# Kernel optimization log

Hardware: AMD Instinct MI355X
Metric: run time of the kernel (lower is better)

The kernel has to match this reference:

```python
import jax, jax.numpy as jnp
import numpy as np

B, C, H, W = 16, 256, 32, 32
AD, SC, R = 16, 32, 4


def _conv1x1(x, w, b):
    # x: [B,Cin,H,W], w: [Cout,Cin], b: [Cout]
    return jnp.einsum('oc,bchw->bohw', w, x) + b[None, :, None, None]


def setup_inputs() -> dict:
    key = jax.random.key(0)
    ks = jax.random.split(key, 12)
    p = lambda k, shape: (jax.random.normal(k, shape, dtype=jnp.float32) * 0.02)
    return {
        'x': jax.random.normal(ks[0], (B, C, H, W), dtype=jnp.float32),
        'fc1_w': p(ks[1], (C // R, C)), 'fc1_b': jnp.zeros((C // R,), jnp.float32),
        'fc2_w': p(ks[2], (C, C // R)), 'fc2_b': jnp.zeros((C,), jnp.float32),
        'qkv_w': p(ks[3], (AD * 2 + SC, SC)), 'qkv_b': jnp.zeros((AD * 2 + SC,), jnp.float32),
        'proj_w': p(ks[4], (SC, SC)), 'proj_b': jnp.zeros((SC,), jnp.float32),
        'ffn1_w': p(ks[5], (4 * C, C)), 'ffn1_b': jnp.zeros((4 * C,), jnp.float32),
        'ffn2_w': p(ks[6], (C, 4 * C)), 'ffn2_b': jnp.zeros((C,), jnp.float32),
    }


def reference(x, fc1_w, fc1_b, fc2_w, fc2_b, qkv_w, qkv_b, proj_w, proj_b,
              ffn1_w, ffn1_b, ffn2_w, ffn2_b):
    # --- DynamicChannelSelect: SE gate then channel split ---
    s = x.mean(axis=(2, 3), keepdims=True)                       # [B,C,1,1]
    s = jax.nn.relu(_conv1x1(s, fc1_w, fc1_b))
    s = jax.nn.sigmoid(_conv1x1(s, fc2_w, fc2_b))
    xg = x * s
    attn_part, non_attn_part = xg[:, :SC], xg[:, SC:]

    # --- SHSA: single-head self-attention on SC channels ---
    qkv = _conv1x1(attn_part, qkv_w, qkv_b)                      # [B,2*AD+SC,H,W]
    q = qkv[:, :AD].reshape(B, AD, H * W)
    k = qkv[:, AD:2 * AD].reshape(B, AD, H * W)
    v = qkv[:, 2 * AD:].reshape(B, SC, H * W)
    scale = AD ** -0.5
    attn = jax.nn.softmax(jnp.einsum('bcn,bcm->bnm', q, k) * scale, axis=-1)  # [B,N,N]
    out = jnp.einsum('bcm,bnm->bcn', v, attn).reshape(B, SC, H, W)
    attn_out = _conv1x1(out, proj_w, proj_b)

    # --- concat + 1x1-conv FFN ---
    y = jnp.concatenate([attn_out, non_attn_part], axis=1)       # [B,C,H,W]
    h = jax.nn.relu(_conv1x1(y, ffn1_w, ffn1_b))                 # [B,4C,H,W]
    return _conv1x1(h, ffn2_w, ffn2_b)                           # [B,C,H,W]
```

## Files before the change

### kernel.cpp

```cpp
#include <hip/hip_runtime.h>
#include <cstdint>
#include <cstddef>

#define BB 16
#define CC 256
#define NP 1024

typedef __attribute__((ext_vector_type(8))) short bf16x8;
typedef __attribute__((ext_vector_type(4))) float f32x4;
typedef unsigned short u16;

__device__ __forceinline__ u16 f2bf(float f) {
    union { float f; uint32_t u; } v; v.f = f;
    uint32_t u = v.u;
    return (u16)((u + 0x7FFFu + ((u >> 16) & 1u)) >> 16);
}

__global__ __launch_bounds__(256)
void se_mean_conv_kernel(const float* __restrict__ x, float* __restrict__ s_mean,
                         const float* __restrict__ w1, u16* __restrict__ d1,
                         const float* __restrict__ w2, u16* __restrict__ d2) {
    int blk = blockIdx.x;
    int t = threadIdx.x;
    if (blk < BB * CC) {
        const float* p = x + (size_t)blk * NP;
        float4 v = *(const float4*)(p + t * 4);
        float s = (v.x + v.y) + (v.z + v.w);
#pragma unroll
        for (int off = 32; off; off >>= 1) s += __shfl_down(s, off, 64);
        __shared__ float red[4];
        if ((t & 63) == 0) red[t >> 6] = s;
        __syncthreads();
        if (t == 0) s_mean[blk] = (red[0] + red[1] + red[2] + red[3]) * (1.0f / NP);
    } else {
        int blk2 = blk - BB * CC;
        const float* src = (blk2 < 256) ? w1 : w2;
        u16* dst = (blk2 < 256) ? d1 : d2;
        int i = ((blk2 & 255) * 256 + t) * 4;
        float4 v = *(const float4*)(src + i);
        ushort4 o;
        o.x = f2bf(v.x); o.y = f2bf(v.y); o.z = f2bf(v.z); o.w = f2bf(v.w);
        *(ushort4*)(dst + i) = o;
    }
}

__global__ __launch_bounds__(256)
void se_mlp_kernel(const float* __restrict__ s_mean,
                   const float* __restrict__ fc1_w, const float* __restrict__ fc1_b,
                   const float* __restrict__ fc2_w, const float* __restrict__ fc2_b,
                   float* __restrict__ sig) {
    int b = blockIdx.x, t = threadIdx.x;
    __shared__ float sm[256];
    __shared__ float part[4][64];
    __shared__ float h1[64];
    sm[t] = s_mean[b * 256 + t];
    __syncthreads();
    int to = t & 63, g = t >> 6;
    float a = 0.f;
#pragma unroll 8
    for (int c = 0; c < 64; ++c) a += fc1_w[to * 256 + g * 64 + c] * sm[g * 64 + c];
    part[g][to] = a;
    __syncthreads();
    if (t < 64) h1[t] = fmaxf(part[0][t] + part[1][t] + part[2][t] + part[3][t] + fc1_b[t], 0.f);
    __syncthreads();
    float acc = fc2_b[t];
#pragma unroll 8
    for (int j = 0; j < 64; ++j) acc += fc2_w[t * 64 + j] * h1[j];
    sig[b * 256 + t] = 1.f / (1.f + __expf(-acc));
}

__global__ __launch_bounds__(256)
void scale_transpose_qkv_kernel(const float* __restrict__ x, const float* __restrict__ sig,
                                const float* __restrict__ qW, const float* __restrict__ qB,
                                u16* __restrict__ ygt, u16* __restrict__ Qt,
                                u16* __restrict__ Kt, u16* __restrict__ Vb) {
    int nt = blockIdx.x, ct = blockIdx.y, b = blockIdx.z;
    __shared__ float tile[64][65];
    __shared__ float ws[64 * 32];
    __shared__ float bs[64];
    __shared__ float vtile[32][64];
    __shared__ float sig_l[64];
    int t = threadIdx.x;
    const float* Xb = x + ((size_t)b * CC + ct * 64) * NP + nt * 64;
    if (t < 64) sig_l[t] = sig[b * 256 + ct * 64 + t];
    if (ct == 0) {
        for (int e = t; e < 2048; e += 256) ws[e] = qW[e];
        if (t < 64) bs[t] = qB[t];
    }
#pragma unroll
    for (int p = 0; p < 4; ++p) {
        int e = t + p * 256;
        int c = e >> 4, n4 = (e & 15) * 4;
        float4 v = *(const float4*)&Xb[(size_t)c * NP + n4];
        tile[c][n4] = v.x; tile[c][n4 + 1] = v.y; tile[c][n4 + 2] = v.z; tile[c][n4 + 3] = v.w;
    }
    __syncthreads();
    u16* Yb = ygt + ((size_t)b * NP + nt * 64) * CC + ct * 64;
#pragma unroll
    for (int p = 0; p < 4; ++p) {
        int e = t + p * 256;
        int n = e >> 4, c4 = (e & 15) * 4;
        if (ct * 64 + c4 >= 32) {
            ushort4 o;
            o.x = f2bf(tile[c4][n] * sig_l[c4]);
            o.y = f2bf(tile[c4 + 1][n] * sig_l[c4 + 1]);
            o.z = f2bf(tile[c4 + 2][n] * sig_l[c4 + 2]);
            o.w = f2bf(tile[c4 + 3][n] * sig_l[c4 + 3]);
            *(ushort4*)&Yb[(size_t)n * CC + c4] = o;
        }
    }
    if (ct == 0) {
        int nn = t & 63, g = t >> 6;
        int n = nt * 64 + nn;
        float xs[32];
#pragma unroll
        for (int c = 0; c < 32; ++c) xs[c] = tile[c][nn] * sig_l[c];
        float acc[16];
#pragma unroll
        for (int oc = 0; oc < 16; ++oc) {
            int o = g * 16 + oc;
            float a = bs[o];
#pragma unroll
            for (int c = 0; c < 32; ++c) a += ws[o * 32 + c] * xs[c];
            acc[oc] = a;
        }
        if (g == 0) {
            u16* qr = Qt + ((size_t)b * NP + n) * 32;
            ushort4 z4; z4.x = 0; z4.y = 0; z4.z = 0; z4.w = 0;
#pragma unroll
            for (int j = 0; j < 16; j += 4) {
                ushort4 o4;
                o4.x = f2bf(acc[j] * 0.25f);     o4.y = f2bf(acc[j + 1] * 0.25f);
                o4.z = f2bf(acc[j + 2] * 0.25f); o4.w = f2bf(acc[j + 3] * 0.25f);
                *(ushort4*)&qr[j] = o4;
            }
            *(ushort4*)&qr[16] = z4; *(ushort4*)&qr[20] = z4;
            *(ushort4*)&qr[24] = z4; *(ushort4*)&qr[28] = z4;
        } else if (g == 1) {
            u16* kr = Kt + ((size_t)b * NP + n) * 32;
            ushort4 z4; z4.x = 0; z4.y = 0; z4.z = 0; z4.w = 0;
#pragma unroll
            for (int j = 0; j < 16; j += 4) {
                ushort4 k4;
                k4.x = f2bf(acc[j]);     k4.y = f2bf(acc[j + 1]);
                k4.z = f2bf(acc[j + 2]); k4.w = f2bf(acc[j + 3]);
                *(ushort4*)&kr[j] = k4;
            }
            *(ushort4*)&kr[16] = z4; *(ushort4*)&kr[20] = z4;
            *(ushort4*)&kr[24] = z4; *(ushort4*)&kr[28] = z4;
        } else {
#pragma unroll
            for (int oc = 0; oc < 16; ++oc) vtile[(g - 2) * 16 + oc][nn] = acc[oc];
        }
        __syncthreads();
        for (int e = t; e < 2048; e += 256) {
            int c = e >> 6, nn2 = e & 63;
            Vb[(size_t)b * 32 * NP + (size_t)c * NP + nt * 64 + nn2] = f2bf(vtile[c][nn2]);
        }
    }
}

__global__ __launch_bounds__(256)
void attn_mfma_kernel(const u16* __restrict__ Qt, const u16* __restrict__ Kt,
                      const u16* __restrict__ Vb,
                      const float* __restrict__ proj_w, const float* __restrict__ proj_b,
                      u16* __restrict__ ygt) {
    int b = blockIdx.x & 15;
    int n0 = (blockIdx.x >> 4) * 16;
    __shared__ __align__(16) u16 P_lds[4][16][40];
    __shared__ float al_lds[4][16];
    __shared__ float sm_lds[4][16];
    __shared__ float sl_lds[4][16];
    __shared__ float O_lds[4][16][33];
    __shared__ float pw_s[32][33];
    __shared__ float pb_s[32];
    int t = threadIdx.x;
    int w = t >> 6, lane = t & 63;
    int q = lane >> 4, idx = lane & 15;

    for (int e = t; e < 1024; e += 256) pw_s[e >> 5][e & 31] = proj_w[e];
    if (t < 32) pb_s[t] = proj_b[t];
    __syncthreads();

    const u16* Qb = Qt + (size_t)b * NP * 32;
    const u16* Kb = Kt + (size_t)b * NP * 32;
    const u16* Vp = Vb + (size_t)b * 32 * NP;

    int nrow = n0 + idx;
    bf16x8 aq = *(const bf16x8*)&Qb[(size_t)nrow * 32 + q * 8];

    f32x4 O0 = {0.f, 0.f, 0.f, 0.f}, O1 = {0.f, 0.f, 0.f, 0.f};
    float m_run[4] = {-1e30f, -1e30f, -1e30f, -1e30f};
    float l_run[4] = {0.f, 0.f, 0.f, 0.f};

    int mbase = w * 256;
    for (int m0 = mbase; m0 < mbase + 256; m0 += 32) {
        bf16x8 bk0 = *(const bf16x8*)&Kb[(size_t)(m0 + idx) * 32 + q * 8];
        bf16x8 bk1 = *(const bf16x8*)&Kb[(size_t)(m0 + 16 + idx) * 32 + q * 8];
        bf16x8 va0 = *(const bf16x8*)&Vp[(size_t)idx * NP + m0 + q * 8];
        bf16x8 va1 = *(const bf16x8*)&Vp[(size_t)(16 + idx) * NP + m0 + q * 8];
        f32x4 z = {0.f, 0.f, 0.f, 0.f};
        f32x4 S0 = __builtin_amdgcn_mfma_f32_16x16x32_bf16(aq, bk0, z, 0, 0, 0);
        f32x4 S1 = __builtin_amdgcn_mfma_f32_16x16x32_bf16(aq, bk1, z, 0, 0, 0);
        float mx[4], p0[4], p1[4], alpha[4];
#pragma unroll
        for (int r = 0; r < 4; ++r) mx[r] = fmaxf(S0[r], S1[r]);
#pragma unroll
        for (int off = 1; off < 16; off <<= 1)
#pragma unroll
            for (int r = 0; r < 4; ++r) mx[r] = fmaxf(mx[r], __shfl_xor(mx[r], off, 64));
#pragma unroll
        for (int r = 0; r < 4; ++r) {
            float nm = fmaxf(m_run[r], mx[r]);
            alpha[r] = __expf(m_run[r] - nm);
            m_run[r] = nm;
            p0[r] = __expf(S0[r] - nm);
            p1[r] = __expf(S1[r] - nm);
        }
#pragma unroll
        for (int r = 0; r < 4; ++r) {
            float s = p0[r] + p1[r];
#pragma unroll
            for (int off = 1; off < 16; off <<= 1) s += __shfl_xor(s, off, 64);
            l_run[r] = l_run[r] * alpha[r] + s;
        }
#pragma unroll
        for (int r = 0; r < 4; ++r) {
            P_lds[w][q * 4 + r][idx]      = f2bf(p0[r]);
            P_lds[w][q * 4 + r][idx + 16] = f2bf(p1[r]);
        }
        if (idx == 0) {
#pragma unroll
            for (int r = 0; r < 4; ++r) al_lds[w][q * 4 + r] = alpha[r];
        }
        float an = al_lds[w][idx];
#pragma unroll
        for (int r = 0; r < 4; ++r) { O0[r] *= an; O1[r] *= an; }
        bf16x8 pf = *(const bf16x8*)&P_lds[w][idx][q * 8];
        O0 = __builtin_amdgcn_mfma_f32_16x16x32_bf16(va0, pf, O0, 0, 0, 0);
        O1 = __builtin_amdgcn_mfma_f32_16x16x32_bf16(va1, pf, O1, 0, 0, 0);
    }
    if (idx == 0) {
#pragma unroll
        for (int r = 0; r < 4; ++r) {
            sm_lds[w][q * 4 + r] = m_run[r];
            sl_lds[w][q * 4 + r] = l_run[r];
        }
    }
#pragma unroll
    for (int r = 0; r < 4; ++r) {
        O_lds[w][idx][q * 4 + r]      = O0[r];
        O_lds[w][idx][q * 4 + r + 16] = O1[r];
    }
    __syncthreads();

#pragma unroll
    for (int p = 0; p < 2; ++p) {
        int el = t + p * 256;
        int row = el >> 5, col = el & 31;
        float m0_ = sm_lds[0][row], m1 = sm_lds[1][row], m2 = sm_lds[2][row], m3 = sm_lds[3][row];
        float gm = fmaxf(fmaxf(m0_, m1), fmaxf(m2, m3));
        float e0 = __expf(m0_ - gm), e1 = __expf(m1 - gm);
        float e2 = __expf(m2 - gm), e3 = __expf(m3 - gm);
        float linv = 1.f / (sl_lds[0][row] * e0 + sl_lds[1][row] * e1 +
                            sl_lds[2][row] * e2 + sl_lds[3][row] * e3);
        O_lds[0][row][col] = (O_lds[0][row][col] * e0 + O_lds[1][row][col] * e1 +
                              O_lds[2][row][col] * e2 + O_lds[3][row][col] * e3) * linv;
    }
    __syncthreads();

    {
        int row = (w << 2) + q;
        float o0 = pb_s[idx], o1 = pb_s[idx + 16];
#pragma unroll
        for (int c = 0; c < 32; ++c) {
            float xv = O_lds[0][row][c];
            o0 += pw_s[idx][c] * xv;
            o1 += pw_s[idx + 16][c] * xv;
        }
        u16* yrow = ygt + ((size_t)b * NP + n0 + row) * CC;
        yrow[idx]      = f2bf(o0);
        yrow[idx + 16] = f2bf(o1);
    }
}

__global__ __launch_bounds__(512, 2)
void ffn_fused_kernel(const u16* __restrict__ w1b, const u16* __restrict__ w2b,
                      const u16* __restrict__ ygt,
                      const float* __restrict__ bias1, const float* __restrict__ bias2,
                      float* __restrict__ out) {
    __shared__ __align__(16) u16 Ys[4][64][64];
    __shared__ __align__(16) u16 Hs[2][64][64];
    __shared__ __align__(16) u16 W2s[2][256][64];
    __shared__ float Bs1[1024];
    int t = threadIdx.x;
    int w = t >> 6, lane = t & 63;
    int q = lane >> 4, idx = lane & 15;
    int srow = lane >> 3;
    int gch = (lane & 7) ^ srow;
    int n0 = blockIdx.x * 64;
    int rot = blockIdx.x & 7;
    int hh = w >> 2, wm = w & 3;

#define ISSUE_W2S(sc_)                                                                     \
    {                                                                                      \
        _Pragma("unroll")                                                                  \
        for (int e = 0; e < 8; ++e) {                                                      \
            int hh2 = e >> 2, rnd = e & 3;                                                 \
            int rw = rnd * 64 + w * 8;                                                     \
            __builtin_amdgcn_global_load_lds(                                              \
                (const __attribute__((address_space(1))) void*)(w2b + (size_t)(rw + srow) * 1024 + (sc_) * 128 + hh2 * 64 + gch * 8), \
                (__attribute__((address_space(3))) void*)(&W2s[hh2][rw][0]),               \
                16, 0, 0);                                                                 \
        }                                                                                  \
    }

#define LOAD_AF(dst, sc_)                                                                  \
    {                                                                                      \
        const u16* a1 = w1b + ((size_t)((sc_) * 128 + w * 16 + idx)) * CC;                 \
        _Pragma("unroll")                                                                  \
        for (int s = 0; s < 8; ++s) dst[s] = *(const bf16x8*)(a1 + s * 32 + q * 8);        \
    }

#pragma unroll
    for (int e = 0; e < 4; ++e) {
        __builtin_amdgcn_global_load_lds(
            (const __attribute__((address_space(1))) void*)(ygt + (size_t)(n0 + w * 8 + srow) * CC + e * 64 + gch * 8),
            (__attribute__((address_space(3))) void*)(&Ys[e][w * 8][0]),
            16, 0, 0);
    }
    Bs1[t] = bias1[t];
    Bs1[t + 512] = bias1[t + 512];

    f32x4 oacc[4][4];
#pragma unroll
    for (int f = 0; f < 4; ++f)
#pragma unroll
        for (int j = 0; j < 4; ++j) { f32x4 z = {0.f, 0.f, 0.f, 0.f}; oacc[f][j] = z; }

    ISSUE_W2S(rot)
    bf16x8 af[8];
    LOAD_AF(af, rot)
    __syncthreads();

    for (int it = 0; it < 8; ++it) {
        int sc  = (it + rot) & 7;
        int scn = (it + 1 + rot) & 7;
        bf16x8 afn[8];
        if (it + 1 < 8) LOAD_AF(afn, scn)

        f32x4 hacc[4];
#pragma unroll
        for (int j = 0; j < 4; ++j) { f32x4 z = {0.f, 0.f, 0.f, 0.f}; hacc[j] = z; }
#pragma unroll
        for (int s = 0; s < 8; ++s) {
            int kb = s >> 1, h2 = s & 1;
#pragma unroll
            for (int j = 0; j < 4; ++j) {
                bf16x8 yb = *(const bf16x8*)&Ys[kb][j * 16 + idx][(((q + 4 * h2) ^ (idx & 7)) * 8)];
                hacc[j] = __builtin_amdgcn_mfma_f32_16x16x32_bf16(af[s], yb, hacc[j], 0, 0, 0);
            }
        }

        int mb = sc * 128 + w * 16 + q * 4;
        float b0 = Bs1[mb], b1v = Bs1[mb + 1], b2v = Bs1[mb + 2], b3v = Bs1[mb + 3];
        int chk_hi = wm * 2 + (q >> 1);
#pragma unroll
        for (int j = 0; j < 4; ++j) {
            int n = j * 16 + idx;
            int chk = chk_hi ^ (n & 7);
            uint32_t lo = (uint32_t)f2bf(fmaxf(hacc[j][0] + b0, 0.f)) |
                          ((uint32_t)f2bf(fmaxf(hacc[j][1] + b1v, 0.f)) << 16);
            uint32_t hi = (uint32_t)f2bf(fmaxf(hacc[j][2] + b2v, 0.f)) |
                          ((uint32_t)f2bf(fmaxf(hacc[j][3] + b3v, 0.f)) << 16);
            uint32_t* hp = (uint32_t*)&Hs[hh][n][chk * 8 + (q & 1) * 4];
            hp[0] = lo; hp[1] = hi;
        }
        __syncthreads();

#pragma unroll
        for (int s2 = 0; s2 < 2; ++s2) {
            bf16x8 a2f[4];
#pragma unroll
            for (int f = 0; f < 4; ++f)
                a2f[f] = *(const bf16x8*)&W2s[hh][wm * 64 + f * 16 + idx][(((q + 4 * s2) ^ (idx & 7)) * 8)];
#pragma unroll
            for (int j = 0; j < 4; ++j) {
                bf16x8 hb = *(const bf16x8*)&Hs[hh][j * 16 + idx][(((q + 4 * s2) ^ (idx & 7)) * 8)];
#pragma unroll
                for (int f = 0; f < 4; ++f)
                    oacc[f][j] = __builtin_amdgcn_mfma_f32_16x16x32_bf16(a2f[f], hb, oacc[f][j], 0, 0, 0);
            }
        }
        __syncthreads();

        if (it + 1 < 8) {
            ISSUE_W2S(scn)
#pragma unroll
            for (int s = 0; s < 8; ++s) af[s] = afn[s];
        }
    }
#undef ISSUE_W2S
#undef LOAD_AF

    float* R = (float*)&W2s[0][0][0];
    if (w >= 4) {
#pragma unroll
        for (int f = 0; f < 4; ++f)
#pragma unroll
            for (int j = 0; j < 4; ++j)
#pragma unroll
                for (int r = 0; r < 4; ++r)
                    R[(wm * 64 + f * 16 + q * 4 + r) * 64 + j * 16 + idx] = oacc[f][j][r];
    }
    __syncthreads();
    if (w < 4) {
        int b = n0 >> 10, nnb = n0 & 1023;
#pragma unroll
        for (int f = 0; f < 4; ++f) {
            int m2 = wm * 64 + f * 16 + q * 4;
            float c0 = bias2[m2], c1 = bias2[m2 + 1], c2 = bias2[m2 + 2], c3 = bias2[m2 + 3];
#pragma unroll
            for (int j = 0; j < 4; ++j) {
                int col = j * 16 + idx;
                const float* Rp = &R[m2 * 64 + col];
                float* p = out + ((size_t)b * CC + m2) * NP + nnb + col;
                f32x4 v = oacc[f][j];
                p[0]      = v.x + c0 + Rp[0];
                p[NP]     = v.y + c1 + Rp[64];
                p[2 * NP] = v.z + c2 + Rp[128];
                p[3 * NP] = v.w + c3 + Rp[192];
            }
        }
    }
}

extern "C" void kernel_launch(void* const* d_in, const int* in_sizes, int n_in,
                              void* d_out, int out_size, void* d_ws, size_t ws_size,
                              hipStream_t stream) {
    const float* x      = (const float*)d_in[0];
    const float* fc1_w  = (const float*)d_in[1];
    const float* fc1_b  = (const float*)d_in[2];
    const float* fc2_w  = (const float*)d_in[3];
    const float* fc2_b  = (const float*)d_in[4];
    const float* qkv_w  = (const float*)d_in[5];
    const float* qkv_b  = (const float*)d_in[6];
    const float* proj_w = (const float*)d_in[7];
    const float* proj_b = (const float*)d_in[8];
    const float* ffn1_w = (const float*)d_in[9];
    const float* ffn1_b = (const float*)d_in[10];
    const float* ffn2_w = (const float*)d_in[11];
    const float* ffn2_b = (const float*)d_in[12];
    float* out = (float*)d_out;

    u16* w1b = (u16*)d_ws;
    u16* w2b = w1b + 262144;
    u16* ygt = w2b + 262144;
    u16* scratch = ygt + (size_t)BB * NP * CC;
    float* s_mean = (float*)scratch;
    float* sig    = s_mean + BB * CC;
    u16* Qt = (u16*)(sig + BB * CC);
    u16* Kt = Qt + (size_t)BB * NP * 32;
    u16* Vb = Kt + (size_t)BB * NP * 32;

    se_mean_conv_kernel<<<BB * CC + 512, 256, 0, stream>>>(x, s_mean, ffn1_w, w1b, ffn2_w, w2b);
    se_mlp_kernel<<<BB, 256, 0, stream>>>(s_mean, fc1_w, fc1_b, fc2_w, fc2_b, sig);
    scale_transpose_qkv_kernel<<<dim3(16, 4, BB), 256, 0, stream>>>(
        x, sig, qkv_w, qkv_b, ygt, Qt, Kt, Vb);
    attn_mfma_kernel<<<BB * 64, 256, 0, stream>>>(Qt, Kt, Vb, proj_w, proj_b, ygt);

    ffn_fused_kernel<<<256, 512, 0, stream>>>(w1b, w2b, ygt, ffn1_b, ffn2_b, out);
}
```

Baseline: 161.3 us.

## Retile FFN1 warp work to 32x32 and prefetch W1 fragments after H barrier

Each warp now computes a 32-row by 32-column tile of the first FFN GEMM (two W1 row groups against half the pixels) instead of 16 rows by all 64 pixels. This halves the Y fragment LDS reads per MFMA, since each Y fragment now feeds two MFMAs. The next chunk's W1 fragments are loaded right after the H barrier, behind a scheduling barrier, rather than before the first GEMM, so the double-buffered afn registers are no longer needed. The cost is that W1 global load latency now has to be hidden by the second GEMM alone. Register pressure from the af array stays about the same.

```diff
diff --git a/kernel.cpp b/kernel.cpp
--- a/kernel.cpp
+++ b/kernel.cpp
@@ -301,6 +301,7 @@
     int n0 = blockIdx.x * 64;
     int rot = blockIdx.x & 7;
     int hh = w >> 2, wm = w & 3;
+    int nh = hh * 32;
 
 #define ISSUE_W2S(sc_)                                                                     \
     {                                                                                      \
@@ -315,11 +316,14 @@
         }                                                                                  \
     }
 
-#define LOAD_AF(dst, sc_)                                                                  \
+#define LOAD_AF(sc_)                                                                       \
     {                                                                                      \
-        const u16* a1 = w1b + ((size_t)((sc_) * 128 + w * 16 + idx)) * CC;                 \
+        const u16* a1 = w1b + ((size_t)((sc_) * 128 + wm * 32 + idx)) * CC;                \
         _Pragma("unroll")                                                                  \
-        for (int s = 0; s < 8; ++s) dst[s] = *(const bf16x8*)(a1 + s * 32 + q * 8);        \
+        for (int i2 = 0; i2 < 2; ++i2)                                                     \
+            _Pragma("unroll")                                                              \
+            for (int s = 0; s < 8; ++s)                                                    \
+                af[i2][s] = *(const bf16x8*)(a1 + (size_t)i2 * 16 * CC + s * 32 + q * 8);  \
     }
 
 #pragma unroll
@@ -339,44 +343,55 @@
         for (int j = 0; j < 4; ++j) { f32x4 z = {0.f, 0.f, 0.f, 0.f}; oacc[f][j] = z; }
 
     ISSUE_W2S(rot)
-    bf16x8 af[8];
-    LOAD_AF(af, rot)
+    bf16x8 af[2][8];
+    LOAD_AF(rot)
     __syncthreads();
 
     for (int it = 0; it < 8; ++it) {
         int sc  = (it + rot) & 7;
         int scn = (it + 1 + rot) & 7;
-        bf16x8 afn[8];
-        if (it + 1 < 8) LOAD_AF(afn, scn)
-
-        f32x4 hacc[4];
-#pragma unroll
-        for (int j = 0; j < 4; ++j) { f32x4 z = {0.f, 0.f, 0.f, 0.f}; hacc[j] = z; }
+
+        f32x4 hacc[2][2];
+#pragma unroll
+        for (int i2 = 0; i2 < 2; ++i2)
+#pragma unroll
+            for (int j = 0; j < 2; ++j) { f32x4 z = {0.f, 0.f, 0.f, 0.f}; hacc[i2][j] = z; }
 #pragma unroll
         for (int s = 0; s < 8; ++s) {
             int kb = s >> 1, h2 = s & 1;
 #pragma unroll
-            for (int j = 0; j < 4; ++j) {
-                bf16x8 yb = *(const bf16x8*)&Ys[kb][j * 16 + idx][(((q + 4 * h2) ^ (idx & 7)) * 8)];
-                hacc[j] = __builtin_amdgcn_mfma_f32_16x16x32_bf16(af[s], yb, hacc[j], 0, 0, 0);
-            }
-        }
-
-        int mb = sc * 128 + w * 16 + q * 4;
-        float b0 = Bs1[mb], b1v = Bs1[mb + 1], b2v = Bs1[mb + 2], b3v = Bs1[mb + 3];
-        int chk_hi = wm * 2 + (q >> 1);
-#pragma unroll
-        for (int j = 0; j < 4; ++j) {
-            int n = j * 16 + idx;
-            int chk = chk_hi ^ (n & 7);
-            uint32_t lo = (uint32_t)f2bf(fmaxf(hacc[j][0] + b0, 0.f)) |
-                          ((uint32_t)f2bf(fmaxf(hacc[j][1] + b1v, 0.f)) << 16);
-            uint32_t hi = (uint32_t)f2bf(fmaxf(hacc[j][2] + b2v, 0.f)) |
-                          ((uint32_t)f2bf(fmaxf(hacc[j][3] + b3v, 0.f)) << 16);
-            uint32_t* hp = (uint32_t*)&Hs[hh][n][chk * 8 + (q & 1) * 4];
-            hp[0] = lo; hp[1] = hi;
+            for (int j = 0; j < 2; ++j) {
+                bf16x8 yb = *(const bf16x8*)&Ys[kb][nh + j * 16 + idx][(((q + 4 * h2) ^ (idx & 7)) * 8)];
+                hacc[0][j] = __builtin_amdgcn_mfma_f32_16x16x32_bf16(af[0][s], yb, hacc[0][j], 0, 0, 0);
+                hacc[1][j] = __builtin_amdgcn_mfma_f32_16x16x32_bf16(af[1][s], yb, hacc[1][j], 0, 0, 0);
+            }
+        }
+
+#pragma unroll
+        for (int i2 = 0; i2 < 2; ++i2) {
+            int u = wm * 2 + i2;
+            int mb = sc * 128 + u * 16 + q * 4;
+            float b0 = Bs1[mb], b1v = Bs1[mb + 1], b2v = Bs1[mb + 2], b3v = Bs1[mb + 3];
+            int hh2 = u >> 2;
+            int g8 = (u & 3) * 2 + (q >> 1);
+#pragma unroll
+            for (int j = 0; j < 2; ++j) {
+                int n = nh + j * 16 + idx;
+                int chk = g8 ^ (n & 7);
+                uint32_t lo = (uint32_t)f2bf(fmaxf(hacc[i2][j][0] + b0, 0.f)) |
+                              ((uint32_t)f2bf(fmaxf(hacc[i2][j][1] + b1v, 0.f)) << 16);
+                uint32_t hi = (uint32_t)f2bf(fmaxf(hacc[i2][j][2] + b2v, 0.f)) |
+                              ((uint32_t)f2bf(fmaxf(hacc[i2][j][3] + b3v, 0.f)) << 16);
+                uint32_t* hp = (uint32_t*)&Hs[hh2][n][chk * 8 + (q & 1) * 4];
+                hp[0] = lo; hp[1] = hi;
+            }
         }
         __syncthreads();
+
+        if (it + 1 < 8) {
+            LOAD_AF(scn)
+            __builtin_amdgcn_sched_barrier(0);
+        }
 
 #pragma unroll
         for (int s2 = 0; s2 < 2; ++s2) {
@@ -394,11 +409,7 @@
         }
         __syncthreads();
 
-        if (it + 1 < 8) {
-            ISSUE_W2S(scn)
-#pragma unroll
-            for (int s = 0; s < 8; ++s) af[s] = afn[s];
-        }
+        if (it + 1 < 8) ISSUE_W2S(scn)
     }
 #undef ISSUE_W2S
 #undef LOAD_AF
```

Measured after the change: 177.3 us. 9.9% more time.
